# Kernel tuning notes

Measured on AMD Instinct MI355X. Metric: run time of the kernel, lower is better.

## Reference

```python
import jax, jax.numpy as jnp
import numpy as np

H, C = 3, 64          # heads, out_channels
NEG_SLOPE = 0.2       # PyG GATConv leaky_relu default
LN_EPS = 1e-5


def setup_inputs() -> dict:
    key = jax.random.key(0)
    ks = jax.random.split(key, 20)
    N, E, D_in, edge_dim = 50000, 800000, 64, 5
    g = lambda k, shape: (jax.random.normal(k, shape, dtype=jnp.float32) * 0.1)
    return {
        "x": jax.random.normal(ks[0], (N, D_in), dtype=jnp.float32),
        "edge_attr": jax.random.normal(ks[1], (E, edge_dim), dtype=jnp.float32),
        "lin_w": g(ks[2], (D_in, H * C)),          # GATConv.lin (bias=False)
        "att_src": g(ks[3], (H, C)),
        "att_dst": g(ks[4], (H, C)),
        "lin_edge_w": g(ks[5], (edge_dim, H * C)),  # GATConv.lin_edge (bias=False)
        "att_edge": g(ks[6], (H, C)),
        "gat_bias": jnp.zeros((H * C,), jnp.float32),
        "w1": g(ks[7], (H * C, C)),
        "b1": jnp.zeros((C,), jnp.float32),
        "ln1_g": jnp.ones((C,), jnp.float32),
        "ln1_b": jnp.zeros((C,), jnp.float32),
        "w2": g(ks[8], (C, C)),
        "b2": jnp.zeros((C,), jnp.float32),
        "ln2_g": jnp.ones((C,), jnp.float32),
        "ln2_b": jnp.zeros((C,), jnp.float32),
        "edge_index": jax.random.randint(ks[9], (2, E), 0, N),
    }


def layer_norm(x, g, b):
    m = jnp.mean(x, axis=-1, keepdims=True)
    v = jnp.mean((x - m) ** 2, axis=-1, keepdims=True)
    return (x - m) * jax.lax.rsqrt(v + LN_EPS) * g + b


def gat_conv(x, edge_index, edge_attr, lin_w, att_src, att_dst,
             lin_edge_w, att_edge, gat_bias):
    N = x.shape[0]
    src, dst = edge_index[0], edge_index[1]

    # add_self_loops=True with fill_value='mean': self-loop edge_attr is the
    # per-node mean of incoming edge attributes (0 if node has no in-edges).
    attr_sum = jax.ops.segment_sum(edge_attr, dst, num_segments=N)       # [N, edge_dim]
    cnt = jax.ops.segment_sum(jnp.ones((dst.shape[0],), edge_attr.dtype), dst, num_segments=N)
    loop_attr = attr_sum / jnp.maximum(cnt, 1.0)[:, None]
    loop = jnp.arange(N, dtype=src.dtype)
    src = jnp.concatenate([src, loop])
    dst = jnp.concatenate([dst, loop])
    ea = jnp.concatenate([edge_attr, loop_attr], axis=0)                  # [E2, edge_dim]

    xs = (x @ lin_w).reshape(N, H, C)                                     # [N, H, C]
    a_src = jnp.einsum('nhc,hc->nh', xs, att_src)                         # [N, H]
    a_dst = jnp.einsum('nhc,hc->nh', xs, att_dst)                         # [N, H]
    e = (ea @ lin_edge_w).reshape(-1, H, C)                               # [E2, H, C]
    a_edge = jnp.einsum('ehc,hc->eh', e, att_edge)                        # [E2, H]

    logits = a_src[src] + a_dst[dst] + a_edge                             # [E2, H]
    logits = jnp.where(logits >= 0, logits, NEG_SLOPE * logits)           # leaky_relu

    # segment softmax over incoming edges of each dst node (self loops ensure non-empty)
    lmax = jax.ops.segment_max(logits, dst, num_segments=N)               # [N, H]
    ex = jnp.exp(logits - lmax[dst])
    denom = jax.ops.segment_sum(ex, dst, num_segments=N)                  # [N, H]
    alpha = ex / denom[dst]                                               # [E2, H]

    msgs = alpha[:, :, None] * xs[src]                                    # [E2, H, C]
    out = jax.ops.segment_sum(msgs, dst, num_segments=N)                  # [N, H, C]
    return out.reshape(N, H * C) + gat_bias


def reference(x, edge_attr, lin_w, att_src, att_dst, lin_edge_w, att_edge,
              gat_bias, w1, b1, ln1_g, ln1_b, w2, b2, ln2_g, ln2_b, edge_index):
    x_gat = gat_conv(x, edge_index, edge_attr, lin_w, att_src, att_dst,
                     lin_edge_w, att_edge, gat_bias)
    x_gat = x_gat @ w1 + b1                         # linear1: [N, C]
    x_gat = layer_norm(x + x_gat, ln1_g, ln1_b)     # layerNorm1(x + x_gat)
    lin = x_gat @ w2 + b2                           # linear2
    out = layer_norm(lin + x_gat, ln2_g, ln2_b)     # layerNorm2(lin + x_gat)
    return out                                      # dropout p=0 -> identity
```

## Files before the change

kernel.cpp:

```cpp
#include <hip/hip_runtime.h>


#define HH 3
#define CC 64
#define DIN 64
#define ED 5
#define HC 192
#define NEG_SLOPE 0.2f
#define LN_EPS 1e-5f
#define LOG2E 1.44269504f

typedef __attribute__((ext_vector_type(8))) short bf16x8;
typedef __attribute__((ext_vector_type(4))) float f32x4;

__device__ __forceinline__ float leaky(float l) { return (l >= 0.f) ? l : NEG_SLOPE * l; }

__device__ __forceinline__ unsigned short f2bf(float f) {
    unsigned u = __float_as_uint(f);
    unsigned r = (u + 0x7FFFu + ((u >> 16) & 1u)) >> 16;
    return (unsigned short)r;
}
__device__ __forceinline__ float bf_lo(unsigned v) { return __uint_as_float(v << 16); }
__device__ __forceinline__ float bf_hi(unsigned v) { return __uint_as_float(v & 0xFFFF0000u); }

__device__ __forceinline__ bf16x8 pack8(float4 a, float4 b) {
    bf16x8 r;
    r[0] = (short)f2bf(a.x); r[1] = (short)f2bf(a.y);
    r[2] = (short)f2bf(a.z); r[3] = (short)f2bf(a.w);
    r[4] = (short)f2bf(b.x); r[5] = (short)f2bf(b.y);
    r[6] = (short)f2bf(b.z); r[7] = (short)f2bf(b.w);
    return r;
}

#define PREP_TOT (HC*DIN + DIN*HC + CC*CC + CC + ED*HH)
#define PREP_BLOCKS 30
__global__ __launch_bounds__(256) void k_prep_cnt(const float* __restrict__ lin_w,
                                                  const float* __restrict__ w1,
                                                  const float* __restrict__ w2,
                                                  const float* __restrict__ b1,
                                                  const float* __restrict__ gat_bias,
                                                  const float* __restrict__ lin_edge_w,
                                                  const float* __restrict__ att_edge,
                                                  unsigned short* __restrict__ linwt,
                                                  unsigned short* __restrict__ w1t,
                                                  unsigned short* __restrict__ w2t,
                                                  float* __restrict__ b1p,
                                                  float* __restrict__ we,
                                                  const int* __restrict__ ei,
                                                  int* __restrict__ icnt, int E) {
    if (blockIdx.x < PREP_BLOCKS) {
        for (int i = blockIdx.x * 256 + threadIdx.x; i < PREP_TOT; i += PREP_BLOCKS * 256) {
            if (i < HC * DIN) {
                int c = i >> 6, k = i & 63;
                linwt[i] = f2bf(lin_w[k * HC + c]);
            } else if (i < 2 * HC * DIN) {
                int j = i - HC * DIN;
                int c = j / HC, k = j - c * HC;
                w1t[j] = f2bf(w1[k * CC + c]);
            } else if (i < 2 * HC * DIN + CC * CC) {
                int j = i - 2 * HC * DIN;
                int c = j >> 6, k = j & 63;
                w2t[j] = f2bf(w2[k * CC + c]);
            } else if (i < 2 * HC * DIN + CC * CC + CC) {
                int c = i - (2 * HC * DIN + CC * CC);
                float s = b1[c];
                for (int k = 0; k < HC; ++k) s += gat_bias[k] * w1[k * CC + c];
                b1p[c] = s;
            } else {
                int q = i - (2 * HC * DIN + CC * CC + CC);
                int d = q / HH, h = q - d * HH;
                float s = 0.f;
                for (int c = 0; c < CC; ++c)
                    s += lin_edge_w[d * HC + h * CC + c] * att_edge[h * CC + c];
                we[q] = s * LOG2E;
            }
        }
    } else {
        int nb = gridDim.x - PREP_BLOCKS;
        for (int e = (blockIdx.x - PREP_BLOCKS) * 256 + threadIdx.x; e < E; e += nb * 256)
            atomicAdd(&icnt[ei[E + e]], 1);
    }
}

__global__ __launch_bounds__(256) void k_xs(const float* __restrict__ x,
                                            const unsigned short* __restrict__ linwt,
                                            const float* __restrict__ att_src,
                                            const float* __restrict__ att_dst,
                                            uint2* __restrict__ xsp,
                                            float* __restrict__ a_src,
                                            float* __restrict__ a_dst, int N) {
    int lane = threadIdx.x & 63, w = threadIdx.x >> 6;
    int l15 = lane & 15, kg = (lane >> 4) * 8;
    int nb = blockIdx.x * 64;
    int arow = nb + w * 16 + l15;
    int arow_c = min(arow, N - 1);

    f32x4 acc[12];
    #pragma unroll
    for (int ct = 0; ct < 12; ++ct) acc[ct] = (f32x4){0.f, 0.f, 0.f, 0.f};

    #pragma unroll
    for (int k0 = 0; k0 < DIN; k0 += 32) {
        const float* ap = x + (size_t)arow_c * DIN + k0 + kg;
        float4 a0 = *(const float4*)ap;
        float4 a1 = *(const float4*)(ap + 4);
        bf16x8 af = pack8(a0, a1);
        #pragma unroll
        for (int ct = 0; ct < 12; ++ct) {
            bf16x8 bf = *(const bf16x8*)(linwt + (size_t)(ct * 16 + l15) * DIN + k0 + kg);
            acc[ct] = __builtin_amdgcn_mfma_f32_16x16x32_bf16(af, bf, acc[ct], 0, 0, 0);
        }
    }

    float asv[12], adv[12];
    #pragma unroll
    for (int ct = 0; ct < 12; ++ct) {
        int c = ct * 16 + l15;
        asv[ct] = att_src[c]; adv[ct] = att_dst[c];
    }

    int rbase = nb + w * 16 + (lane >> 4) * 4;
    #pragma unroll
    for (int j = 0; j < 4; ++j) {
        int r = rbase + j;
        bool ok = r < N;
        float ps0 = 0.f, ps1 = 0.f, ps2 = 0.f, pd0 = 0.f, pd1 = 0.f, pd2 = 0.f;
        #pragma unroll
        for (int ct = 0; ct < 12; ++ct) {
            float v = acc[ct][j];
            float s = v * asv[ct], d = v * adv[ct];
            if (ct < 4)      { ps0 += s; pd0 += d; }
            else if (ct < 8) { ps1 += s; pd1 += d; }
            else             { ps2 += s; pd2 += d; }
        }
        if (ok) {
            #pragma unroll
            for (int ct = 0; ct < 4; ++ct) {
                uint2 pk;
                pk.x = (unsigned)f2bf(acc[ct][j]) | ((unsigned)f2bf(acc[ct + 4][j]) << 16);
                pk.y = (unsigned)f2bf(acc[ct + 8][j]);
                xsp[(size_t)r * CC + ct * 16 + l15] = pk;
            }
        }
        #pragma unroll
        for (int o = 1; o < 16; o <<= 1) {
            ps0 += __shfl_xor(ps0, o, 64); pd0 += __shfl_xor(pd0, o, 64);
            ps1 += __shfl_xor(ps1, o, 64); pd1 += __shfl_xor(pd1, o, 64);
            ps2 += __shfl_xor(ps2, o, 64); pd2 += __shfl_xor(pd2, o, 64);
        }
        if (ok && l15 == 0) {
            a_src[r * HH + 0] = ps0 * LOG2E; a_src[r * HH + 1] = ps1 * LOG2E;
            a_src[r * HH + 2] = ps2 * LOG2E;
            a_dst[r * HH + 0] = pd0 * LOG2E; a_dst[r * HH + 1] = pd1 * LOG2E;
            a_dst[r * HH + 2] = pd2 * LOG2E;
        }
    }
}

__global__ __launch_bounds__(256) void k_scan1(const int* __restrict__ icnt,
                                               int* __restrict__ bsum, int N) {
    int i = blockIdx.x * 256 + threadIdx.x;
    int lane = threadIdx.x & 63, wid = threadIdx.x >> 6;
    int v = (i < N) ? icnt[i] : 0;
    #pragma unroll
    for (int o = 32; o; o >>= 1) v += __shfl_xor(v, o, 64);
    __shared__ int wt[4];
    if (lane == 0) wt[wid] = v;
    __syncthreads();
    if (threadIdx.x == 0) bsum[blockIdx.x] = wt[0] + wt[1] + wt[2] + wt[3];
}

__global__ __launch_bounds__(1024) void k_scan2(const int* __restrict__ bsum,
                                                int* __restrict__ boff, int nb) {
    __shared__ int s[1024];
    int t = threadIdx.x;
    int v = (t < nb) ? bsum[t] : 0;
    s[t] = v;
    __syncthreads();
    for (int d = 1; d < 1024; d <<= 1) {
        int u = (t >= d) ? s[t - d] : 0;
        __syncthreads();
        s[t] += u;
        __syncthreads();
    }
    if (t < nb) boff[t] = s[t] - v;
}

__global__ __launch_bounds__(256) void k_scan3(const int* __restrict__ icnt,
                                               const int* __restrict__ boff,
                                               int* __restrict__ off,
                                               int* __restrict__ cursor, int N) {
    int i = blockIdx.x * 256 + threadIdx.x;
    int lane = threadIdx.x & 63, wid = threadIdx.x >> 6;
    int v = (i < N) ? icnt[i] : 0;
    int incl = v;
    #pragma unroll
    for (int o = 1; o < 64; o <<= 1) {
        int u = __shfl_up(incl, o, 64);
        if (lane >= o) incl += u;
    }
    __shared__ int wt[4];
    if (lane == 63) wt[wid] = incl;
    __syncthreads();
    int wpre = 0;
    for (int w = 0; w < wid; ++w) wpre += wt[w];
    int excl = boff[blockIdx.x] + wpre + incl - v;
    if (i < N) {
        off[i] = excl;
        cursor[i] = excl;
        if (i == N - 1) off[N] = excl + v;
    }
}

__global__ __launch_bounds__(256) void k_fill(const float* __restrict__ ea,
                                              const int* __restrict__ ei,
                                              const float* __restrict__ a_src,
                                              const float* __restrict__ we,
                                              int* __restrict__ cursor,
                                              uint4* __restrict__ payload, int E) {
    int e = blockIdx.x * blockDim.x + threadIdx.x;
    if (e >= E) return;
    int s = ei[e], d = ei[E + e];
    float attr[ED];
    #pragma unroll
    for (int j = 0; j < ED; ++j) attr[j] = ea[(size_t)e * ED + j];
    float aeh[HH], lp[HH];
    #pragma unroll
    for (int h = 0; h < HH; ++h) {
        float a = 0.f;
        #pragma unroll
        for (int j = 0; j < ED; ++j) a += attr[j] * we[j * HH + h];
        aeh[h] = a;
        lp[h] = a_src[s * HH + h] + a;
    }
    int pos = atomicAdd(&cursor[d], 1);
    uint4 pk;
    pk.x = (unsigned)f2bf(lp[0])  | ((unsigned)f2bf(lp[1])  << 16);
    pk.y = (unsigned)f2bf(lp[2])  | ((unsigned)f2bf(aeh[0]) << 16);
    pk.z = (unsigned)f2bf(aeh[1]) | ((unsigned)f2bf(aeh[2]) << 16);
    pk.w = (unsigned)s;
    payload[pos] = pk;
}

__global__ __launch_bounds__(256) void k_gat(const uint2* __restrict__ xsp,
                                             const float* __restrict__ a_src,
                                             const float* __restrict__ a_dst,
                                             const int* __restrict__ off,
                                             const uint4* __restrict__ payload,
                                             unsigned short* __restrict__ oaccb, int N) {
    __shared__ float4 wbuf[4][64];
    int lane = threadIdx.x & 63;
    int wid  = threadIdx.x >> 6;
    for (int n = blockIdx.x * 4 + wid; n < N; n += gridDim.x * 4) {
        int beg = off[n], end = off[n + 1];
        int deg = end - beg;
        float ad0 = a_dst[n * HH + 0], ad1 = a_dst[n * HH + 1], ad2 = a_dst[n * HH + 2];
        float pden0 = 0.f, pden1 = 0.f, pden2 = 0.f;
        float pae0 = 0.f, pae1 = 0.f, pae2 = 0.f;
        float a0A = 0.f, a1A = 0.f, a2A = 0.f;
        float a0B = 0.f, a1B = 0.f, a2B = 0.f;

        for (int c0 = 0; c0 < deg; c0 += 64) {
            int cn = min(deg - c0, 64);
            float w0 = 0.f, w1 = 0.f, w2 = 0.f;
            int src = 0;
            if (lane < cn) {
                uint4 p = payload[beg + c0 + lane];
                w0 = exp2f(leaky(bf_lo(p.x) + ad0));
                w1 = exp2f(leaky(bf_hi(p.x) + ad1));
                w2 = exp2f(leaky(bf_lo(p.y) + ad2));
                pae0 += bf_hi(p.y);
                pae1 += bf_lo(p.z);
                pae2 += bf_hi(p.z);
                pden0 += w0; pden1 += w1; pden2 += w2;
                src = (int)p.w;
            }
            wbuf[wid][lane] = make_float4(w0, w1, w2, __int_as_float(src));
            int i = 0;
            for (; i + 2 <= cn; i += 2) {
                float4 ta = wbuf[wid][i];
                float4 tb = wbuf[wid][i + 1];
                unsigned ia = (unsigned)__float_as_int(ta.w) * CC + lane;
                unsigned ib = (unsigned)__float_as_int(tb.w) * CC + lane;
                uint2 va = xsp[ia];
                uint2 vb = xsp[ib];
                a0A += ta.x * bf_lo(va.x); a1A += ta.y * bf_hi(va.x); a2A += ta.z * bf_lo(va.y);
                a0B += tb.x * bf_lo(vb.x); a1B += tb.y * bf_hi(vb.x); a2B += tb.z * bf_lo(vb.y);
            }
            if (i < cn) {
                float4 ta = wbuf[wid][i];
                unsigned ia = (unsigned)__float_as_int(ta.w) * CC + lane;
                uint2 va = xsp[ia];
                a0A += ta.x * bf_lo(va.x); a1A += ta.y * bf_hi(va.x); a2A += ta.z * bf_lo(va.y);
            }
        }

        #pragma unroll
        for (int o = 32; o; o >>= 1) {
            pden0 += __shfl_xor(pden0, o, 64);
            pden1 += __shfl_xor(pden1, o, 64);
            pden2 += __shfl_xor(pden2, o, 64);
            pae0  += __shfl_xor(pae0, o, 64);
            pae1  += __shfl_xor(pae1, o, 64);
            pae2  += __shfl_xor(pae2, o, 64);
        }

        float dc = fmaxf((float)deg, 1.0f);
        float inv_dc = 1.0f / dc;
        float sl0 = leaky(a_src[n * HH + 0] + ad0 + pae0 * inv_dc);
        float sl1 = leaky(a_src[n * HH + 1] + ad1 + pae1 * inv_dc);
        float sl2 = leaky(a_src[n * HH + 2] + ad2 + pae2 * inv_dc);
        float e0 = exp2f(sl0), e1 = exp2f(sl1), e2 = exp2f(sl2);
        uint2 vn = xsp[(unsigned)n * CC + lane];
        float den0 = pden0 + e0, den1 = pden1 + e1, den2 = pden2 + e2;
        float acc0 = a0A + a0B + e0 * bf_lo(vn.x);
        float acc1 = a1A + a1B + e1 * bf_hi(vn.x);
        float acc2 = a2A + a2B + e2 * bf_lo(vn.y);
        size_t nbse = (size_t)n * HC;
        oaccb[nbse + 0 * CC + lane] = f2bf(acc0 / den0);
        oaccb[nbse + 1 * CC + lane] = f2bf(acc1 / den1);
        oaccb[nbse + 2 * CC + lane] = f2bf(acc2 / den2);
    }
}

__global__ __launch_bounds__(256) void k_mlp(const unsigned short* __restrict__ oaccb,
                                             const unsigned short* __restrict__ w1t,
                                             const unsigned short* __restrict__ w2t,
                                             const float* __restrict__ b1p,
                                             const float* __restrict__ x,
                                             const float* __restrict__ g1,
                                             const float* __restrict__ be1,
                                             const float* __restrict__ b2,
                                             const float* __restrict__ g2,
                                             const float* __restrict__ be2,
                                             float* __restrict__ out, int N) {
    __shared__ unsigned short H1[64 * 72];
    int lane = threadIdx.x & 63, w = threadIdx.x >> 6;
    int l15 = lane & 15, kg = (lane >> 4) * 8;
    int nb = blockIdx.x * 64;
    int arow = nb + w * 16 + l15;
    int arow_c = min(arow, N - 1);

    float c_b1[4], c_g1[4], c_be1[4], c_b2[4], c_g2[4], c_be2[4];
    #pragma unroll
    for (int ct = 0; ct < 4; ++ct) {
        int c = ct * 16 + l15;
        c_b1[ct] = b1p[c]; c_g1[ct] = g1[c]; c_be1[ct] = be1[c];
        c_b2[ct] = b2[c];  c_g2[ct] = g2[c]; c_be2[ct] = be2[c];
    }

    f32x4 acc[4];
    #pragma unroll
    for (int ct = 0; ct < 4; ++ct) acc[ct] = (f32x4){0.f, 0.f, 0.f, 0.f};
    #pragma unroll
    for (int k0 = 0; k0 < HC; k0 += 32) {
        bf16x8 af = *(const bf16x8*)(oaccb + (size_t)arow_c * HC + k0 + kg);
        #pragma unroll
        for (int ct = 0; ct < 4; ++ct) {
            bf16x8 bf = *(const bf16x8*)(w1t + (size_t)(ct * 16 + l15) * HC + k0 + kg);
            acc[ct] = __builtin_amdgcn_mfma_f32_16x16x32_bf16(af, bf, acc[ct], 0, 0, 0);
        }
    }

    int rbase = nb + w * 16 + (lane >> 4) * 4;
    int rloc0 = w * 16 + (lane >> 4) * 4;
    float h1v[4][4];
    float y[4][4];
    #pragma unroll
    for (int j = 0; j < 4; ++j) {
        int r = min(rbase + j, N - 1);
        #pragma unroll
        for (int ct = 0; ct < 4; ++ct)
            y[ct][j] = acc[ct][j] + c_b1[ct] + x[(size_t)r * DIN + ct * 16 + l15];
    }
    #pragma unroll
    for (int j = 0; j < 4; ++j) {
        float s = y[0][j] + y[1][j] + y[2][j] + y[3][j];
        #pragma unroll
        for (int o = 1; o < 16; o <<= 1) s += __shfl_xor(s, o, 64);
        float m = s * (1.0f / CC);
        float vs = 0.f;
        #pragma unroll
        for (int ct = 0; ct < 4; ++ct) { float d = y[ct][j] - m; vs += d * d; }
        #pragma unroll
        for (int o = 1; o < 16; o <<= 1) vs += __shfl_xor(vs, o, 64);
        float inv = rsqrtf(vs * (1.0f / CC) + LN_EPS);
        #pragma unroll
        for (int ct = 0; ct < 4; ++ct) {
            float h = (y[ct][j] - m) * inv * c_g1[ct] + c_be1[ct];
            h1v[ct][j] = h;
            H1[(rloc0 + j) * 72 + ct * 16 + l15] = f2bf(h);
        }
    }
    __syncthreads();

    f32x4 acc2[4];
    #pragma unroll
    for (int ct = 0; ct < 4; ++ct) acc2[ct] = (f32x4){0.f, 0.f, 0.f, 0.f};
    #pragma unroll
    for (int k0 = 0; k0 < CC; k0 += 32) {
        bf16x8 af = *(const bf16x8*)&H1[(w * 16 + l15) * 72 + k0 + kg];
        #pragma unroll
        for (int ct = 0; ct < 4; ++ct) {
            bf16x8 bf = *(const bf16x8*)(w2t + (size_t)(ct * 16 + l15) * CC + k0 + kg);
            acc2[ct] = __builtin_amdgcn_mfma_f32_16x16x32_bf16(af, bf, acc2[ct], 0, 0, 0);
        }
    }

    #pragma unroll
    for (int j = 0; j < 4; ++j) {
        float z0 = acc2[0][j] + c_b2[0] + h1v[0][j];
        float z1 = acc2[1][j] + c_b2[1] + h1v[1][j];
        float z2 = acc2[2][j] + c_b2[2] + h1v[2][j];
        float z3 = acc2[3][j] + c_b2[3] + h1v[3][j];
        float s = z0 + z1 + z2 + z3;
        #pragma unroll
        for (int o = 1; o < 16; o <<= 1) s += __shfl_xor(s, o, 64);
        float m = s * (1.0f / CC);
        float d0 = z0 - m, d1 = z1 - m, d2 = z2 - m, d3 = z3 - m;
        float vs = d0 * d0 + d1 * d1 + d2 * d2 + d3 * d3;
        #pragma unroll
        for (int o = 1; o < 16; o <<= 1) vs += __shfl_xor(vs, o, 64);
        float inv = rsqrtf(vs * (1.0f / CC) + LN_EPS);
        int r = rbase + j;
        if (r < N) {
            out[(size_t)r * CC + 0 * 16 + l15] = d0 * inv * c_g2[0] + c_be2[0];
            out[(size_t)r * CC + 1 * 16 + l15] = d1 * inv * c_g2[1] + c_be2[1];
            out[(size_t)r * CC + 2 * 16 + l15] = d2 * inv * c_g2[2] + c_be2[2];
            out[(size_t)r * CC + 3 * 16 + l15] = d3 * inv * c_g2[3] + c_be2[3];
        }
    }
}

extern "C" void kernel_launch(void* const* d_in, const int* in_sizes, int n_in,
                              void* d_out, int out_size, void* d_ws, size_t ws_size,
                              hipStream_t stream) {
    const float* x          = (const float*)d_in[0];
    const float* edge_attr  = (const float*)d_in[1];
    const float* lin_w      = (const float*)d_in[2];
    const float* att_src    = (const float*)d_in[3];
    const float* att_dst    = (const float*)d_in[4];
    const float* lin_edge_w = (const float*)d_in[5];
    const float* att_edge   = (const float*)d_in[6];
    const float* gat_bias   = (const float*)d_in[7];
    const float* w1         = (const float*)d_in[8];
    const float* b1         = (const float*)d_in[9];
    const float* ln1_g      = (const float*)d_in[10];
    const float* ln1_b      = (const float*)d_in[11];
    const float* w2         = (const float*)d_in[12];
    const float* b2         = (const float*)d_in[13];
    const float* ln2_g      = (const float*)d_in[14];
    const float* ln2_b      = (const float*)d_in[15];
    const int*   ei         = (const int*)d_in[16];
    float* out = (float*)d_out;

    const int N = in_sizes[0] / DIN;
    const int E = in_sizes[1] / ED;
    const int nb_scan = (N + 255) / 256;

    char* ws = (char*)d_ws;
    size_t off_b = 0;
    auto alloc = [&](size_t bytes) {
        size_t o = off_b;
        off_b = (off_b + bytes + 255) & ~(size_t)255;
        return o;
    };
    int* icnt = (int*)(ws + alloc((size_t)N * 4));
    size_t zero_bytes = off_b;
    uint2* xsp            = (uint2*)(ws + alloc((size_t)N * CC * 8));
    unsigned short* oaccb = (unsigned short*)(ws + alloc((size_t)N * HC * 2));
    float*  a_srcb  = (float*)(ws + alloc((size_t)N * HH * 4));
    float*  a_dstb  = (float*)(ws + alloc((size_t)N * HH * 4));
    int*    offb    = (int*)(ws + alloc((size_t)(N + 1) * 4));
    int*    cursor  = (int*)(ws + alloc((size_t)N * 4));
    int*    bsum    = (int*)(ws + alloc((size_t)nb_scan * 4));
    int*    boff    = (int*)(ws + alloc((size_t)nb_scan * 4));
    uint4*  payload = (uint4*)(ws + alloc((size_t)E * 16));
    unsigned short* linwt = (unsigned short*)(ws + alloc((size_t)HC * DIN * 2));
    unsigned short* w1t   = (unsigned short*)(ws + alloc((size_t)DIN * HC * 2));
    unsigned short* w2t   = (unsigned short*)(ws + alloc((size_t)CC * CC * 2));
    float* b1p = (float*)(ws + alloc((size_t)CC * 4));
    float* we  = (float*)(ws + alloc((size_t)ED * HH * 4));
    (void)ws_size; (void)n_in; (void)out_size;

    hipMemsetAsync(d_ws, 0, zero_bytes, stream);

    k_prep_cnt<<<PREP_BLOCKS + (E + 255) / 256, 256, 0, stream>>>(
        lin_w, w1, w2, b1, gat_bias, lin_edge_w, att_edge,
        linwt, w1t, w2t, b1p, we, ei, icnt, E);
    k_xs<<<(N + 63) / 64, 256, 0, stream>>>(x, linwt, att_src, att_dst, xsp, a_srcb, a_dstb, N);
    k_scan1<<<nb_scan, 256, 0, stream>>>(icnt, bsum, N);
    k_scan2<<<1, 1024, 0, stream>>>(bsum, boff, nb_scan);
    k_scan3<<<nb_scan, 256, 0, stream>>>(icnt, boff, offb, cursor, N);
    k_fill<<<(E + 255) / 256, 256, 0, stream>>>(edge_attr, ei, a_srcb, we, cursor,
                                                payload, E);
    k_gat<<<(N + 3) / 4, 256, 0, stream>>>(xsp, a_srcb, a_dstb, offb, payload, oaccb, N);
    k_mlp<<<(N + 63) / 64, 256, 0, stream>>>(oaccb, w1t, w2t, b1p, x,
                                             ln1_g, ln1_b, b2, ln2_g, ln2_b, out, N);
}
```

Before: 204.0 us.

## Store projected features as dense bf16 rows and unroll gather by four

The padded interleaved uint2 layout (8 bytes per channel, 2 bytes wasted) is replaced by a dense bf16 [N,192] head-major layout, so each gathered source row is 384 bytes instead of 512. The aggregation loop now issues three 2-byte loads per edge rather than one 8-byte load. It is unrolled to four edges with four accumulator sets to expose more loads in flight. The aim is less gather bandwidth and better latency hiding, at the cost of more load instructions and more registers.

```diff
diff --git a/kernel.cpp b/kernel.cpp
--- a/kernel.cpp
+++ b/kernel.cpp
@@ -19,6 +19,9 @@
     unsigned u = __float_as_uint(f);
     unsigned r = (u + 0x7FFFu + ((u >> 16) & 1u)) >> 16;
     return (unsigned short)r;
+}
+__device__ __forceinline__ float bf2f(unsigned short u) {
+    return __uint_as_float((unsigned)u << 16);
 }
 __device__ __forceinline__ float bf_lo(unsigned v) { return __uint_as_float(v << 16); }
 __device__ __forceinline__ float bf_hi(unsigned v) { return __uint_as_float(v & 0xFFFF0000u); }
@@ -86,7 +89,7 @@
                                             const unsigned short* __restrict__ linwt,
                                             const float* __restrict__ att_src,
                                             const float* __restrict__ att_dst,
-                                            uint2* __restrict__ xsp,
+                                            unsigned short* __restrict__ xsb,
                                             float* __restrict__ a_src,
                                             float* __restrict__ a_dst, int N) {
     int lane = threadIdx.x & 63, w = threadIdx.x >> 6;
@@ -128,19 +131,11 @@
         #pragma unroll
         for (int ct = 0; ct < 12; ++ct) {
             float v = acc[ct][j];
+            if (ok) xsb[(size_t)r * HC + ct * 16 + l15] = f2bf(v);
             float s = v * asv[ct], d = v * adv[ct];
             if (ct < 4)      { ps0 += s; pd0 += d; }
             else if (ct < 8) { ps1 += s; pd1 += d; }
             else             { ps2 += s; pd2 += d; }
-        }
-        if (ok) {
-            #pragma unroll
-            for (int ct = 0; ct < 4; ++ct) {
-                uint2 pk;
-                pk.x = (unsigned)f2bf(acc[ct][j]) | ((unsigned)f2bf(acc[ct + 4][j]) << 16);
-                pk.y = (unsigned)f2bf(acc[ct + 8][j]);
-                xsp[(size_t)r * CC + ct * 16 + l15] = pk;
-            }
         }
         #pragma unroll
         for (int o = 1; o < 16; o <<= 1) {
@@ -242,7 +237,7 @@
     payload[pos] = pk;
 }
 
-__global__ __launch_bounds__(256) void k_gat(const uint2* __restrict__ xsp,
+__global__ __launch_bounds__(256) void k_gat(const unsigned short* __restrict__ xsb,
                                              const float* __restrict__ a_src,
                                              const float* __restrict__ a_dst,
                                              const int* __restrict__ off,
@@ -259,6 +254,8 @@
         float pae0 = 0.f, pae1 = 0.f, pae2 = 0.f;
         float a0A = 0.f, a1A = 0.f, a2A = 0.f;
         float a0B = 0.f, a1B = 0.f, a2B = 0.f;
+        float a0C = 0.f, a1C = 0.f, a2C = 0.f;
+        float a0D = 0.f, a1D = 0.f, a2D = 0.f;
 
         for (int c0 = 0; c0 < deg; c0 += 64) {
             int cn = min(deg - c0, 64);
@@ -277,21 +274,34 @@
             }
             wbuf[wid][lane] = make_float4(w0, w1, w2, __int_as_float(src));
             int i = 0;
-            for (; i + 2 <= cn; i += 2) {
+            for (; i + 4 <= cn; i += 4) {
                 float4 ta = wbuf[wid][i];
                 float4 tb = wbuf[wid][i + 1];
-                unsigned ia = (unsigned)__float_as_int(ta.w) * CC + lane;
-                unsigned ib = (unsigned)__float_as_int(tb.w) * CC + lane;
-                uint2 va = xsp[ia];
-                uint2 vb = xsp[ib];
-                a0A += ta.x * bf_lo(va.x); a1A += ta.y * bf_hi(va.x); a2A += ta.z * bf_lo(va.y);
-                a0B += tb.x * bf_lo(vb.x); a1B += tb.y * bf_hi(vb.x); a2B += tb.z * bf_lo(vb.y);
+                float4 tc = wbuf[wid][i + 2];
+                float4 td = wbuf[wid][i + 3];
+                unsigned sa = (unsigned)__float_as_int(ta.w) * HC + lane;
+                unsigned sb = (unsigned)__float_as_int(tb.w) * HC + lane;
+                unsigned sc = (unsigned)__float_as_int(tc.w) * HC + lane;
+                unsigned sd = (unsigned)__float_as_int(td.w) * HC + lane;
+                a0A += ta.x * bf2f(xsb[sa]);
+                a1A += ta.y * bf2f(xsb[sa + 64]);
+                a2A += ta.z * bf2f(xsb[sa + 128]);
+                a0B += tb.x * bf2f(xsb[sb]);
+                a1B += tb.y * bf2f(xsb[sb + 64]);
+                a2B += tb.z * bf2f(xsb[sb + 128]);
+                a0C += tc.x * bf2f(xsb[sc]);
+                a1C += tc.y * bf2f(xsb[sc + 64]);
+                a2C += tc.z * bf2f(xsb[sc + 128]);
+                a0D += td.x * bf2f(xsb[sd]);
+                a1D += td.y * bf2f(xsb[sd + 64]);
+                a2D += td.z * bf2f(xsb[sd + 128]);
             }
-            if (i < cn) {
+            for (; i < cn; ++i) {
                 float4 ta = wbuf[wid][i];
-                unsigned ia = (unsigned)__float_as_int(ta.w) * CC + lane;
-                uint2 va = xsp[ia];
-                a0A += ta.x * bf_lo(va.x); a1A += ta.y * bf_hi(va.x); a2A += ta.z * bf_lo(va.y);
+                unsigned sa = (unsigned)__float_as_int(ta.w) * HC + lane;
+                a0A += ta.x * bf2f(xsb[sa]);
+                a1A += ta.y * bf2f(xsb[sa + 64]);
+                a2A += ta.z * bf2f(xsb[sa + 128]);
             }
         }
 
@@ -311,11 +321,11 @@
         float sl1 = leaky(a_src[n * HH + 1] + ad1 + pae1 * inv_dc);
         float sl2 = leaky(a_src[n * HH + 2] + ad2 + pae2 * inv_dc);
         float e0 = exp2f(sl0), e1 = exp2f(sl1), e2 = exp2f(sl2);
-        uint2 vn = xsp[(unsigned)n * CC + lane];
+        unsigned nb_ = (unsigned)n * HC + lane;
         float den0 = pden0 + e0, den1 = pden1 + e1, den2 = pden2 + e2;
-        float acc0 = a0A + a0B + e0 * bf_lo(vn.x);
-        float acc1 = a1A + a1B + e1 * bf_hi(vn.x);
-        float acc2 = a2A + a2B + e2 * bf_lo(vn.y);
+        float acc0 = a0A + a0B + a0C + a0D + e0 * bf2f(xsb[nb_]);
+        float acc1 = a1A + a1B + a1C + a1D + e1 * bf2f(xsb[nb_ + 64]);
+        float acc2 = a2A + a2B + a2C + a2D + e2 * bf2f(xsb[nb_ + 128]);
         size_t nbse = (size_t)n * HC;
         oaccb[nbse + 0 * CC + lane] = f2bf(acc0 / den0);
         oaccb[nbse + 1 * CC + lane] = f2bf(acc1 / den1);
@@ -467,7 +477,7 @@
     };
     int* icnt = (int*)(ws + alloc((size_t)N * 4));
     size_t zero_bytes = off_b;
-    uint2* xsp            = (uint2*)(ws + alloc((size_t)N * CC * 8));
+    unsigned short* xsb   = (unsigned short*)(ws + alloc((size_t)N * HC * 2));
     unsigned short* oaccb = (unsigned short*)(ws + alloc((size_t)N * HC * 2));
     float*  a_srcb  = (float*)(ws + alloc((size_t)N * HH * 4));
     float*  a_dstb  = (float*)(ws + alloc((size_t)N * HH * 4));
@@ -488,13 +498,13 @@
     k_prep_cnt<<<PREP_BLOCKS + (E + 255) / 256, 256, 0, stream>>>(
         lin_w, w1, w2, b1, gat_bias, lin_edge_w, att_edge,
         linwt, w1t, w2t, b1p, we, ei, icnt, E);
-    k_xs<<<(N + 63) / 64, 256, 0, stream>>>(x, linwt, att_src, att_dst, xsp, a_srcb, a_dstb, N);
+    k_xs<<<(N + 63) / 64, 256, 0, stream>>>(x, linwt, att_src, att_dst, xsb, a_srcb, a_dstb, N);
     k_scan1<<<nb_scan, 256, 0, stream>>>(icnt, bsum, N);
     k_scan2<<<1, 1024, 0, stream>>>(bsum, boff, nb_scan);
     k_scan3<<<nb_scan, 256, 0, stream>>>(icnt, boff, offb, cursor, N);
     k_fill<<<(E + 255) / 256, 256, 0, stream>>>(edge_attr, ei, a_srcb, we, cursor,
                                                 payload, E);
-    k_gat<<<(N + 3) / 4, 256, 0, stream>>>(xsp, a_srcb, a_dstb, offb, payload, oaccb, N);
+    k_gat<<<(N + 3) / 4, 256, 0, stream>>>(xsb, a_srcb, a_dstb, offb, payload, oaccb, N);
     k_mlp<<<(N + 63) / 64, 256, 0, stream>>>(oaccb, w1t, w2t, b1p, x,
                                              ln1_g, ln1_b, b2, ln2_g, ln2_b, out, N);
 }
```

After: 204.7 us. No clear change (+0.3%).
